# Kernel tuning notes

Measured on AMD Instinct MI355X. Metric: run time of the kernel, lower is better.

## Reference

```python
import jax, jax.numpy as jnp
import numpy as np

B, T, C, HS = 4, 4096, 1024, 64  # batch, seq, n_embd, head_size


def setup_inputs() -> dict:
    key = jax.random.key(0)
    kx, kq, kk, kv = jax.random.split(key, 4)
    s = 1.0 / np.sqrt(C)  # Linear-like init scale
    return {
        "x": jax.random.normal(kx, (B, T, C), dtype=jnp.float32),
        "Wq": jax.random.normal(kq, (C, HS), dtype=jnp.float32) * s,
        "bq": jnp.zeros((HS,), dtype=jnp.float32),
        "Wk": jax.random.normal(kk, (C, HS), dtype=jnp.float32) * s,
        "bk": jnp.zeros((HS,), dtype=jnp.float32),
        "Wv": jax.random.normal(kv, (C, HS), dtype=jnp.float32) * s,
        "bv": jnp.zeros((HS,), dtype=jnp.float32),
    }


def reference(x, Wq, bq, Wk, bk, Wv, bv):
    # x: [B,T,C]
    q = x @ Wq + bq          # [B,T,HS]
    k = x @ Wk + bk          # [B,T,HS]
    v = x @ Wv + bv          # [B,T,HS]
    att = jnp.einsum("bqh,bkh->bqk", q, k)  # [B,T,T]
    att = att * (C ** -0.5)  # NOTE: scales by n_embd, not head_size (faithful to source)
    causal = jnp.tril(jnp.ones((T, T), dtype=bool))
    att = jnp.where(causal, att, -jnp.inf)
    att = jax.nn.softmax(att, axis=-1)
    # dropout p=0.0 (eval): identity
    out = jnp.einsum("bqk,bkh->bqh", att, v)  # [B,T,HS]
    return out
```

## Files before the change

### kernel.cpp

```cpp
#include <hip/hip_runtime.h>
#include <hip/hip_bf16.h>
#include <math.h>

#define B 4
#define T 4096
#define C 1024
#define HS 64

typedef __attribute__((ext_vector_type(8))) short short8;
typedef __attribute__((ext_vector_type(4))) float f32x4;
typedef __attribute__((ext_vector_type(16))) float f32x16;

#define MFMA16(a, b, c) __builtin_amdgcn_mfma_f32_16x16x32_bf16((a), (b), (c), 0, 0, 0)
#define MFMA32(a, b, c) __builtin_amdgcn_mfma_f32_32x32x16_bf16((a), (b), (c), 0, 0, 0)

#define QSCALE 0.0450842200278f

static __device__ __forceinline__ unsigned short f2bf(float f) {
  union { float f; unsigned u; } v; v.f = f;
  unsigned r = v.u + 0x7FFFu + ((v.u >> 16) & 1u);
  return (unsigned short)(r >> 16);
}

static __device__ __forceinline__ unsigned pack_bf2(float lo, float hi2) {
  union { __hip_bfloat16 h; unsigned short u; } a, c;
  a.h = __float2bfloat16(lo); c.h = __float2bfloat16(hi2);
  return (unsigned)a.u | ((unsigned)c.u << 16);
}

__global__ __launch_bounds__(256) void conv_w_kernel(
    const float* __restrict__ Wq, const float* __restrict__ Wk,
    const float* __restrict__ Wv, unsigned short* __restrict__ Wt) {
  const int wi = blockIdx.x >> 4;
  const int c0 = (blockIdx.x & 15) * 64;
  const float* W = (wi == 0) ? Wq : (wi == 1) ? Wk : Wv;
  __shared__ float ws[64][65];
  const int t = threadIdx.x;
  const int r = t >> 2;
  const int cb = (t & 3) * 16;
#pragma unroll
  for (int j = 0; j < 4; ++j) {
    const f32x4 v = *(const f32x4*)&W[(size_t)(c0 + r) * HS + cb + 4 * j];
    ws[cb + 4 * j + 0][r] = v[0];
    ws[cb + 4 * j + 1][r] = v[1];
    ws[cb + 4 * j + 2][r] = v[2];
    ws[cb + 4 * j + 3][r] = v[3];
  }
  __syncthreads();
  const int h = t >> 2;
  const int rb = (t & 3) * 16;
  union { short8 s8[2]; unsigned short u[16]; } o;
#pragma unroll
  for (int i = 0; i < 16; ++i) o.u[i] = f2bf(ws[h][rb + i]);
  short8* dst = (short8*)(Wt + (size_t)(wi * 64 + h) * C + c0 + rb);
  dst[0] = o.s8[0];
  dst[1] = o.s8[1];
}

__global__ __launch_bounds__(512, 4) void proj_kernel(
    const float* __restrict__ x, const unsigned short* __restrict__ Wt,
    const float* __restrict__ bq, const float* __restrict__ bk,
    const float* __restrict__ bv,
    unsigned short* __restrict__ Qf, unsigned short* __restrict__ Kf,
    unsigned short* __restrict__ Vf) {
  const int m0   = blockIdx.x * 64;
  const int w    = threadIdx.x >> 6;
  const int lane = threadIdx.x & 63;
  const int col  = lane & 15, grp = lane >> 4;
  const int wm   = w >> 2;
  const int wn   = w & 3;
  const int phase = blockIdx.x & 15;

  __shared__ unsigned short A_lds[2][64 * 64];
  __shared__ unsigned short B_lds[2][24][512];

  const int arow  = threadIdx.x >> 3;
  const int acol8 = threadIdx.x & 7;
  const float* xp = x + (size_t)(m0 + arow) * C + acol8 * 8;

  f32x4 acc[2][3];
#pragma unroll
  for (int mf = 0; mf < 2; ++mf)
#pragma unroll
    for (int jj = 0; jj < 3; ++jj) acc[mf][jj] = (f32x4){0.f, 0.f, 0.f, 0.f};

  auto kcOf = [&](int it) { return ((it + phase) & 15) * 64; };

  auto stageB = [&](int nb, int kc) {
#pragma unroll
    for (int j = 0; j < 3; ++j) {
      const int f   = w * 3 + j;
      const int nt  = f % 12;
      const int k32 = f / 12;
      const unsigned short* src =
          Wt + (size_t)(nt * 16 + col) * C + kc + k32 * 32 + grp * 8;
      __builtin_amdgcn_global_load_lds(
          (const __attribute__((address_space(1))) void*)src,
          (__attribute__((address_space(3))) void*)&B_lds[nb][f][0],
          16, 0, 0);
    }
  };

  auto loadAreg = [&](int kc, f32x4& r0, f32x4& r1) {
    r0 = *(const f32x4*)(xp + kc);
    r1 = *(const f32x4*)(xp + kc + 4);
  };

  auto writeA = [&](int nb, const f32x4& r0, const f32x4& r1) {
    union { short8 s8; unsigned short u[8]; } o;
#pragma unroll
    for (int e = 0; e < 4; ++e) {
      o.u[e] = f2bf(r0[e]);
      o.u[4 + e] = f2bf(r1[e]);
    }
    const int b0 = arow * 128 + acol8 * 16;
    const int s  = (arow & 7) << 4;
    *(short8*)((char*)&A_lds[nb][0] + (b0 ^ s)) = o.s8;
  };

  auto readA = [&](int buf, int mf, int k32) {
    const int row = wm * 32 + mf * 16 + col;
    const int b = row * 128 + ((k32 * 64 + grp * 16) ^ ((col & 7) << 4));
    return *(const short8*)((const char*)&A_lds[buf][0] + b);
  };

  auto compute = [&](int buf) {
#pragma unroll
    for (int k32 = 0; k32 < 2; ++k32) {
      const short8 a0 = readA(buf, 0, k32);
      const short8 a1 = readA(buf, 1, k32);
#pragma unroll
      for (int jj = 0; jj < 3; ++jj) {
        const short8 bf =
            *(const short8*)&B_lds[buf][k32 * 12 + wn * 3 + jj][(size_t)lane * 8];
        acc[0][jj] = MFMA16(a0, bf, acc[0][jj]);
        acc[1][jj] = MFMA16(a1, bf, acc[1][jj]);
      }
    }
  };

  f32x4 aR0, aR1;
  loadAreg(kcOf(0), aR0, aR1);
  stageB(0, kcOf(0));
  writeA(0, aR0, aR1);
  loadAreg(kcOf(1), aR0, aR1);
  __syncthreads();

  for (int it = 0; it < 16; ++it) {
    const int buf = it & 1;
    if (it < 15) stageB(buf ^ 1, kcOf(it + 1));
    compute(buf);
    if (it < 15) {
      writeA(buf ^ 1, aR0, aR1);
      if (it < 14) loadAreg(kcOf(it + 2), aR0, aR1);
    }
    __syncthreads();
  }

  auto writeOut = [&](int row, int n, float v) {
    const int bb  = row >> 12;
    const int t   = row & (T - 1);
    const int blk = t >> 5;
    const int r   = t & 31;
    if (n < 64) {
      const int j = n >> 4, h2 = (n >> 3) & 1, e = n & 7;
      Qf[((((size_t)bb * 128 + blk) * 4 + j) * 64 + h2 * 32 + r) * 8 + e] =
          f2bf(v * QSCALE);
    } else if (n < 128) {
      const int d = n - 64;
      const int f = d >> 4, h2 = (d >> 3) & 1, e = d & 7;
      Kf[((((size_t)bb * 128 + blk) * 4 + f) * 64 + h2 * 32 + r) * 8 + e] =
          f2bf(v);
    } else {
      const int d = n - 128;
      const int e = r & 7, h2 = (r >> 3) & 1, half = (r >> 4) & 1;
      const int vi = ((d >> 5) << 1) + half;
      const int q = d & 31;
      Vf[((((size_t)bb * 128 + blk) * 4 + vi) * 64 + h2 * 32 + q) * 8 + e] =
          f2bf(v);
    }
  };
#pragma unroll
  for (int mf = 0; mf < 2; ++mf) {
#pragma unroll
    for (int jj = 0; jj < 3; ++jj) {
      const int n = wn * 48 + jj * 16 + col;
      const float bias = (n < 64) ? bq[n] : (n < 128) ? bk[n - 64] : bv[n - 128];
#pragma unroll
      for (int r = 0; r < 4; ++r)
        writeOut(m0 + wm * 32 + mf * 16 + 4 * grp + r, n, acc[mf][jj][r] + bias);
    }
  }
}

__global__ __launch_bounds__(512, 2) void attn_kernel(
    const unsigned short* __restrict__ Qf,
    const unsigned short* __restrict__ Kf,
    const unsigned short* __restrict__ Vf,
    float* __restrict__ out) {
  const int x8 = blockIdx.x & 7;
  const int b  = x8 >> 1;
  const int p  = ((blockIdx.x >> 3) << 1) | (x8 & 1);

  const int w8   = threadIdx.x >> 6;
  const int g    = w8 >> 2;
  const int w    = w8 & 3;
  const int lane = threadIdx.x & 63;
  const int q    = lane & 31;
  const int hi   = lane >> 5;
  const int qt   = g ? (127 - p) : p;
  const int qbase = qt * 32;
  const int qg    = qbase + q;

  __shared__ float accL[8][64][33];
  __shared__ float lL[8][32], invL[2][32];

  const unsigned short* Qp = Qf + ((size_t)(b * 128 + qt) * 4) * 512;
  const unsigned short* Kb = Kf + ((size_t)b * 128) * 4 * 512;
  const unsigned short* Vb = Vf + ((size_t)b * 128) * 4 * 512;

  short8 qf[4];
#pragma unroll
  for (int j = 0; j < 4; ++j)
    qf[j] = *(const short8*)(Qp + j * 512 + lane * 8);

  f32x16 acc0, acc1;
#pragma unroll
  for (int r = 0; r < 16; ++r) { acc0[r] = 0.f; acc1[r] = 0.f; }
  float lsum = 0.f;

  const int nkv = qt + 1;

  short8 kA[4], vA[4], kB[4], vB[4];

  auto loadKV = [&](int kb, short8 (&kd)[4], short8 (&vd)[4]) {
    const unsigned short* pk = Kb + (size_t)kb * 2048 + lane * 8;
    kd[0] = *(const short8*)(pk);
    kd[1] = *(const short8*)(pk + 512);
    kd[2] = *(const short8*)(pk + 1024);
    kd[3] = *(const short8*)(pk + 1536);
    const unsigned short* pv = Vb + (size_t)kb * 2048 + lane * 8;
    vd[0] = *(const short8*)(pv);
    vd[1] = *(const short8*)(pv + 512);
    vd[2] = *(const short8*)(pv + 1024);
    vd[3] = *(const short8*)(pv + 1536);
  };

  auto step = [&](int kb, short8 (&kc)[4], short8 (&vc)[4],
                  short8 (&kn)[4], short8 (&vn)[4]) {
    int knb = kb + 4;
    if (knb > 127) knb = 127;
    loadKV(knb, kn, vn);

    f32x16 s;
#pragma unroll
    for (int r = 0; r < 16; ++r) s[r] = -8.0f;
    s = MFMA32(kc[0], qf[0], s);
    s = MFMA32(kc[1], qf[1], s);
    s = MFMA32(kc[2], qf[2], s);
    s = MFMA32(kc[3], qf[3], s);

    float pe[16];
    if (kb == qt) {
      const int qrel = qg - kb * 32;
#pragma unroll
      for (int r = 0; r < 16; ++r) {
        const int key = (r & 3) + 8 * (r >> 2) + 4 * hi;
        const float v = exp2f(s[r]);
        pe[r] = (key <= qrel) ? v : 0.f;
      }
    } else {
#pragma unroll
      for (int r = 0; r < 16; ++r) pe[r] = exp2f(s[r]);
    }
#pragma unroll
    for (int r = 0; r < 16; ++r) lsum += pe[r];

    unsigned own[8], oth[8];
#pragma unroll
    for (int j = 0; j < 8; ++j) own[j] = pack_bf2(pe[2 * j], pe[2 * j + 1]);
#pragma unroll
    for (int j = 0; j < 8; ++j) oth[j] = __shfl_xor(own[j], 32, 64);
    union U { short8 s8; unsigned u[4]; };
    U p0, p1;
    p0.u[0] = hi ? oth[2] : own[0];
    p0.u[1] = hi ? oth[3] : own[1];
    p0.u[2] = hi ? own[2] : oth[0];
    p0.u[3] = hi ? own[3] : oth[1];
    p1.u[0] = hi ? oth[6] : own[4];
    p1.u[1] = hi ? oth[7] : own[5];
    p1.u[2] = hi ? own[6] : oth[4];
    p1.u[3] = hi ? own[7] : oth[5];

    acc0 = MFMA32(vc[0], p0.s8, acc0);
    acc0 = MFMA32(vc[1], p1.s8, acc0);
    acc1 = MFMA32(vc[2], p0.s8, acc1);
    acc1 = MFMA32(vc[3], p1.s8, acc1);
  };

  if (w < nkv) {
    loadKV(w, kA, vA);
    int kb = w;
    while (true) {
      step(kb, kA, vA, kB, vB); kb += 4; if (kb >= nkv) break;
      step(kb, kB, vB, kA, vA); kb += 4; if (kb >= nkv) break;
    }
  }

  lsum += __shfl_xor(lsum, 32, 64);
  if (hi == 0) lL[w8][q] = lsum;
#pragma unroll
  for (int r = 0; r < 16; ++r) {
    const int d = (r & 3) + 8 * (r >> 2) + 4 * hi;
    accL[w8][d][q]      = acc0[r];
    accL[w8][d + 32][q] = acc1[r];
  }
  __syncthreads();
  if (threadIdx.x < 64) {
    const int g2 = threadIdx.x >> 5;
    const int qq = threadIdx.x & 31;
    const float L = lL[g2 * 4 + 0][qq] + lL[g2 * 4 + 1][qq] +
                    lL[g2 * 4 + 2][qq] + lL[g2 * 4 + 3][qq];
    invL[g2][qq] = 1.f / L;
  }
  __syncthreads();
  {
    const int tid2 = threadIdx.x & 255;
#pragma unroll
    for (int pp = 0; pp < 8; ++pp) {
      const int qq = (tid2 >> 6) + 4 * pp;
      const int d  = tid2 & 63;
      const float v = accL[g * 4 + 0][d][qq] + accL[g * 4 + 1][d][qq] +
                      accL[g * 4 + 2][d][qq] + accL[g * 4 + 3][d][qq];
      out[(size_t)(b * T + qbase + qq) * HS + d] = v * invL[g][qq];
    }
  }
}

extern "C" void kernel_launch(void* const* d_in, const int* in_sizes, int n_in,
                              void* d_out, int out_size, void* d_ws, size_t ws_size,
                              hipStream_t stream) {
  const float* x  = (const float*)d_in[0];
  const float* Wq = (const float*)d_in[1];
  const float* bq = (const float*)d_in[2];
  const float* Wk = (const float*)d_in[3];
  const float* bk = (const float*)d_in[4];
  const float* Wv = (const float*)d_in[5];
  const float* bv = (const float*)d_in[6];
  float* out = (float*)d_out;

  unsigned short* Qf = (unsigned short*)d_ws;
  unsigned short* Kf = Qf + (size_t)B * T * HS;
  unsigned short* Vf = Kf + (size_t)B * T * HS;
  unsigned short* Wt = Vf + (size_t)B * T * HS;

  conv_w_kernel<<<48, 256, 0, stream>>>(Wq, Wk, Wv, Wt);
  proj_kernel<<<B * T / 64, 512, 0, stream>>>(x, Wt, bq, bk, bv, Qf, Kf, Vf);
  attn_kernel<<<B * 64, 512, 0, stream>>>(Qf, Kf, Vf, out);
}
```

Measured before the change: 57.28 us.

## Pre-tile weights into MFMA fragment layout and rebalance attention warps by causal work

The weight conversion kernel now writes the bf16 weights directly in the per-fragment tiled order that proj_kernel stages into LDS, so each wave's global-to-LDS load reads one contiguous 1 KiB chunk instead of strided rows. In the attention kernel, the 8 waves are no longer split 4/4 between the short and long causal query tiles. They are divided in proportion to each tile's key-block count, which aims to reduce imbalance between the two halves of the block. The reduction loops become variable-length over the wave ranges, adding some index math and non-unrolled loops.

```diff
diff --git a/kernel.cpp b/kernel.cpp
--- a/kernel.cpp
+++ b/kernel.cpp
@@ -30,7 +30,7 @@
 
 __global__ __launch_bounds__(256) void conv_w_kernel(
     const float* __restrict__ Wq, const float* __restrict__ Wk,
-    const float* __restrict__ Wv, unsigned short* __restrict__ Wt) {
+    const float* __restrict__ Wv, unsigned short* __restrict__ Wtf) {
   const int wi = blockIdx.x >> 4;
   const int c0 = (blockIdx.x & 15) * 64;
   const float* W = (wi == 0) ? Wq : (wi == 1) ? Wk : Wv;
@@ -47,18 +47,28 @@
     ws[cb + 4 * j + 3][r] = v[3];
   }
   __syncthreads();
-  const int h = t >> 2;
+  const int h  = t >> 2;
   const int rb = (t & 3) * 16;
-  union { short8 s8[2]; unsigned short u[16]; } o;
-#pragma unroll
-  for (int i = 0; i < 16; ++i) o.u[i] = f2bf(ws[h][rb + i]);
-  short8* dst = (short8*)(Wt + (size_t)(wi * 64 + h) * C + c0 + rb);
-  dst[0] = o.s8[0];
-  dst[1] = o.s8[1];
+  const int n   = wi * 64 + h;
+  const int nt  = n >> 4;
+  const int col = n & 15;
+#pragma unroll
+  for (int j = 0; j < 2; ++j) {
+    const int cbase = c0 + rb + j * 8;
+    union { short8 s8; unsigned short u[8]; } o;
+#pragma unroll
+    for (int e = 0; e < 8; ++e) o.u[e] = f2bf(ws[h][rb + j * 8 + e]);
+    const int kc128 = cbase >> 7;
+    const int k32   = (cbase >> 5) & 3;
+    const int grp   = (cbase >> 3) & 3;
+    const size_t idx =
+        ((size_t)(kc128 * 48 + k32 * 12 + nt) * 512 + (grp * 16 + col) * 8);
+    *(short8*)(Wtf + idx) = o.s8;
+  }
 }
 
 __global__ __launch_bounds__(512, 4) void proj_kernel(
-    const float* __restrict__ x, const unsigned short* __restrict__ Wt,
+    const float* __restrict__ x, const unsigned short* __restrict__ Wtf,
     const float* __restrict__ bq, const float* __restrict__ bk,
     const float* __restrict__ bv,
     unsigned short* __restrict__ Qf, unsigned short* __restrict__ Kf,
@@ -87,16 +97,18 @@
   auto kcOf = [&](int it) { return ((it + phase) & 15) * 64; };
 
   auto stageB = [&](int nb, int kc) {
+    const int kc128 = kc >> 7;
+    const int k32b  = (kc >> 5) & 3;
 #pragma unroll
     for (int j = 0; j < 3; ++j) {
-      const int f   = w * 3 + j;
-      const int nt  = f % 12;
-      const int k32 = f / 12;
+      const int fl  = w * 3 + j;
+      const int nt  = fl % 12;
+      const int k32 = k32b + fl / 12;
       const unsigned short* src =
-          Wt + (size_t)(nt * 16 + col) * C + kc + k32 * 32 + grp * 8;
+          Wtf + ((size_t)(kc128 * 48 + k32 * 12 + nt) * 512) + lane * 8;
       __builtin_amdgcn_global_load_lds(
           (const __attribute__((address_space(1))) void*)src,
-          (__attribute__((address_space(3))) void*)&B_lds[nb][f][0],
+          (__attribute__((address_space(3))) void*)&B_lds[nb][fl][0],
           16, 0, 0);
     }
   };
@@ -203,8 +215,13 @@
   const int p  = ((blockIdx.x >> 3) << 1) | (x8 & 1);
 
   const int w8   = threadIdx.x >> 6;
-  const int g    = w8 >> 2;
-  const int w    = w8 & 3;
+  const int n0   = p + 1;
+  int w0 = (8 * n0 + 64) / 129;
+  if (w0 < 1) w0 = 1;
+  if (w0 > 7) w0 = 7;
+  const int g    = (w8 >= w0) ? 1 : 0;
+  const int lw   = g ? (w8 - w0) : w8;
+  const int nw   = g ? (8 - w0) : w0;
   const int lane = threadIdx.x & 63;
   const int q    = lane & 31;
   const int hi   = lane >> 5;
@@ -248,7 +265,7 @@
 
   auto step = [&](int kb, short8 (&kc)[4], short8 (&vc)[4],
                   short8 (&kn)[4], short8 (&vn)[4]) {
-    int knb = kb + 4;
+    int knb = kb + nw;
     if (knb > 127) knb = 127;
     loadKV(knb, kn, vn);
 
@@ -298,12 +315,12 @@
     acc1 = MFMA32(vc[3], p1.s8, acc1);
   };
 
-  if (w < nkv) {
-    loadKV(w, kA, vA);
-    int kb = w;
+  if (lw < nkv) {
+    loadKV(lw, kA, vA);
+    int kb = lw;
     while (true) {
-      step(kb, kA, vA, kB, vB); kb += 4; if (kb >= nkv) break;
-      step(kb, kB, vB, kA, vA); kb += 4; if (kb >= nkv) break;
+      step(kb, kA, vA, kB, vB); kb += nw; if (kb >= nkv) break;
+      step(kb, kB, vB, kA, vA); kb += nw; if (kb >= nkv) break;
     }
   }
 
@@ -319,20 +336,24 @@
   if (threadIdx.x < 64) {
     const int g2 = threadIdx.x >> 5;
     const int qq = threadIdx.x & 31;
-    const float L = lL[g2 * 4 + 0][qq] + lL[g2 * 4 + 1][qq] +
-                    lL[g2 * 4 + 2][qq] + lL[g2 * 4 + 3][qq];
+    const int lo = g2 ? w0 : 0, hiW = g2 ? 8 : w0;
+    float L = 0.f;
+    for (int ww = lo; ww < hiW; ++ww) L += lL[ww][qq];
     invL[g2][qq] = 1.f / L;
   }
   __syncthreads();
   {
+    const int ge   = threadIdx.x >> 8;
     const int tid2 = threadIdx.x & 255;
+    const int qbE  = (ge ? (127 - p) : p) * 32;
+    const int lo = ge ? w0 : 0, hiW = ge ? 8 : w0;
 #pragma unroll
     for (int pp = 0; pp < 8; ++pp) {
       const int qq = (tid2 >> 6) + 4 * pp;
       const int d  = tid2 & 63;
-      const float v = accL[g * 4 + 0][d][qq] + accL[g * 4 + 1][d][qq] +
-                      accL[g * 4 + 2][d][qq] + accL[g * 4 + 3][d][qq];
-      out[(size_t)(b * T + qbase + qq) * HS + d] = v * invL[g][qq];
+      float v = 0.f;
+      for (int ww = lo; ww < hiW; ++ww) v += accL[ww][d][qq];
+      out[(size_t)(b * T + qbE + qq) * HS + d] = v * invL[ge][qq];
     }
   }
 }
@@ -349,12 +370,12 @@
   const float* bv = (const float*)d_in[6];
   float* out = (float*)d_out;
 
-  unsigned short* Qf = (unsigned short*)d_ws;
-  unsigned short* Kf = Qf + (size_t)B * T * HS;
-  unsigned short* Vf = Kf + (size_t)B * T * HS;
-  unsigned short* Wt = Vf + (size_t)B * T * HS;
-
-  conv_w_kernel<<<48, 256, 0, stream>>>(Wq, Wk, Wv, Wt);
-  proj_kernel<<<B * T / 64, 512, 0, stream>>>(x, Wt, bq, bk, bv, Qf, Kf, Vf);
+  unsigned short* Qf  = (unsigned short*)d_ws;
+  unsigned short* Kf  = Qf + (size_t)B * T * HS;
+  unsigned short* Vf  = Kf + (size_t)B * T * HS;
+  unsigned short* Wtf = Vf + (size_t)B * T * HS;
+
+  conv_w_kernel<<<48, 256, 0, stream>>>(Wq, Wk, Wv, Wtf);
+  proj_kernel<<<B * T / 64, 512, 0, stream>>>(x, Wtf, bq, bk, bv, Qf, Kf, Vf);
   attn_kernel<<<B * 64, 512, 0, stream>>>(Qf, Kf, Vf, out);
 }
```

After: 54.89 us. 4.2% less time.
